# Performance work log

Hardware: AMD Instinct MI355X
Metric: run time of the kernel (lower is better)

## Reference

```python
import jax, jax.numpy as jnp
import numpy as np

B, T, E, K, NNEG = 128, 512, 128, 4, 64


def setup_inputs() -> dict:
    key = jax.random.key(0)
    k1, k2, k3, k4 = jax.random.split(key, 4)
    base_payload = jax.random.normal(k1, (B, T, E), dtype=jnp.float32)
    mapped_ctx_payload = jax.random.normal(k2, (B, T, E, K), dtype=jnp.float32)
    seq_lens = jax.random.randint(k3, (B,), 1, T + 1, dtype=jnp.int32)
    # valid positions mask over the flattened (B*T) pool of possible negatives
    valid = (jnp.arange(T)[None, :] < seq_lens[:, None]).reshape(-1)  # [B*T]
    logits = jnp.where(valid, 0.0, -1e30)[None, :]                    # [1, B*T]
    logits = jnp.broadcast_to(logits, (B, B * T))
    # mirrors torch.multinomial(mask, n_negatives): one draw set per batch row
    sample_ids = jax.random.categorical(k4, logits, shape=(NNEG, B)).T.astype(jnp.int32)
    return {
        "base_payload": base_payload,
        "mapped_ctx_payload": mapped_ctx_payload,
        "seq_lens": seq_lens,
        "sample_ids": sample_ids,
    }


def reference(base_payload, mapped_ctx_payload, seq_lens, sample_ids):
    b, t, e = base_payload.shape
    n_steps = mapped_ctx_payload.shape[-1]
    # length mask [b, t]
    len_mask = (jnp.arange(t)[None, :] < seq_lens[:, None]).astype(base_payload.dtype)
    # zero context embeddings past each sequence's length
    trimmed_mce = mapped_ctx_payload * len_mask[:, :, None, None]  # [b, t, e, n_steps]
    # gather sampled negatives from the flattened base embedding pool
    neg_samples = base_payload.reshape(b * t, e)[sample_ids]  # [b, n_neg, e]

    step_losses = []
    for i in range(1, n_steps + 1):
        ce_i = trimmed_mce[:, : t - i, :, i - 1]   # [b, t-i, e]
        be_i = base_payload[:, i:]                  # [b, t-i, e]
        positive_pred = jnp.sum(ce_i * be_i, axis=-1)             # [b, t-i]
        neg_pred = jnp.einsum('bse,bne->bsn', ce_i, neg_samples)  # [b, t-i, n_neg]
        logits = jnp.concatenate([positive_pred[..., None], neg_pred], axis=-1)
        step_losses.append(-jax.nn.log_softmax(logits, axis=-1)[:, :, 0].mean())
    return jnp.stack(step_losses).mean()
```

## Files before the change

### kernel.cpp

```cpp
#include <hip/hip_runtime.h>
#include <math.h>

#define NB 128
#define NT 512
#define NEDIM 128
#define NNEG 64
#define SCHUNK 16
#define CPB 4
#define SBLK (SCHUNK * CPB)
#define NXBLK (NT / SBLK)
#define NBLKS (NB * NXBLK)
#define WSN (NBLKS * 4)

typedef __bf16 bf16x8 __attribute__((ext_vector_type(8)));
typedef float  f32x4  __attribute__((ext_vector_type(4)));

__device__ __forceinline__ bf16x8 pack8(float4 v0, float4 v1) {
    bf16x8 o;
    o[0] = (__bf16)v0.x; o[1] = (__bf16)v0.y; o[2] = (__bf16)v0.z; o[3] = (__bf16)v0.w;
    o[4] = (__bf16)v1.x; o[5] = (__bf16)v1.y; o[6] = (__bf16)v1.z; o[7] = (__bf16)v1.w;
    return o;
}

__device__ __forceinline__ float chunk_const(int s0c) {
    const float wgt[4] = {1.f/261632.f, 1.f/261120.f, 1.f/260608.f, 1.f/260096.f};
    const float LOG65 = 4.1743873f;
    float c = 0.f;
    #pragma unroll
    for (int i = 1; i <= 4; ++i) {
        int hi = min(SCHUNK, (NT - i) - s0c);
        if (hi > 0) c += (float)hi * LOG65 * wgt[i - 1];
    }
    return c;
}

__launch_bounds__(256, 2)
__global__ void cpc_mfma_kernel(const float* __restrict__ base,
                                const float* __restrict__ mce,
                                const int*  __restrict__ seq_lens,
                                const int*  __restrict__ sample_ids,
                                float* __restrict__ ws)
{
    const int b    = blockIdx.y;
    const int s0   = blockIdx.x * SBLK;
    const int slot = (b * NXBLK + blockIdx.x) * 4;
    const int L    = seq_lens[b];
    const float LOG65 = 4.1743873f;
    const float wgt[4] = {1.f/261632.f, 1.f/261120.f, 1.f/260608.f, 1.f/260096.f};

    if (s0 >= L) {
        if (threadIdx.x < 4) {
            float c = 0.f;
            if (threadIdx.x == 0) {
                #pragma unroll
                for (int cc = 0; cc < CPB; ++cc) c += chunk_const(s0 + cc * SCHUNK);
            }
            ws[slot + threadIdx.x] = c;
        }
        return;
    }

    __shared__ __align__(16) __bf16 Afrag[2][1024 * 8];
    __shared__ __align__(16) __bf16 Bfrag[1024 * 8];
    __shared__ __align__(16) __bf16 Pfrag[2][512 * 8];

    const int tid  = threadIdx.x;
    const int lane = tid & 63;
    const int w    = tid >> 6;
    const int q    = lane >> 4;
    const int fl   = lane & 15;

    const float4* mce4  = (const float4*)mce;
    const float4* base4 = (const float4*)base;

    #pragma unroll
    for (int it = 0; it < 4; ++it) {
        int h  = tid + 256 * it;
        int n  = h >> 4;
        int eb = h & 15;
        int r  = sample_ids[b * NNEG + n];
        const float4* srcb = base4 + (size_t)r * (NEDIM / 4) + eb * 2;
        float4 v0 = srcb[0], v1 = srcb[1];
        *(bf16x8*)(&Bfrag[(size_t)((eb * 64 + n) ^ (eb & 7)) * 8]) = pack8(v0, v1);
    }

    const int sA  = tid & 15;
    const int ebA = tid >> 4;
    const int CsS = (ebA >> 2) * 4 + (sA >> 2);
    const int bcA = CsS * 64 + (ebA & 3) * 16 + (sA & 3) * 4;
    const int xA  = CsS & 7;

    {
        const float4* src = mce4 + (size_t)(b * NT + s0 + sA) * NEDIM + ebA * 8;
        float4 v[8];
        #pragma unroll
        for (int u = 0; u < 8; ++u) v[u] = src[u];
        const float* vf = (const float*)v;
        #pragma unroll
        for (int k = 0; k < 4; ++k) {
            bf16x8 o;
            #pragma unroll
            for (int u = 0; u < 8; ++u) o[u] = (__bf16)vf[4 * u + k];
            *(bf16x8*)(&Afrag[0][(size_t)((bcA + k) ^ xA) * 8]) = o;
        }
        #pragma unroll
        for (int it = 0; it < 2; ++it) {
            int h = tid + 256 * it;
            int j = h >> 4, ebP = h & 15;
            int srow = s0 + 1 + j; if (srow > NT - 1) srow = NT - 1;
            const float4* srcp = base4 + (size_t)(b * NT + srow) * (NEDIM / 4) + ebP * 2;
            *(bf16x8*)(&Pfrag[0][(size_t)((ebP * 32 + j) ^ (ebP & 7)) * 8]) = pack8(srcp[0], srcp[1]);
        }
    }
    __syncthreads();

    float lossacc = 0.f;
    const int sloc = w * 4 + q;

    for (int c = 0; c < CPB; ++c) {
        const int s0c = s0 + c * SCHUNK;
        const bool vcur  = (s0c < L);
        const bool vnext = (c + 1 < CPB) && (s0 + (c + 1) * SCHUNK < L);

        float4 av[8];
        float4 pv0a, pv0b, pv1a, pv1b;
        if (vnext) {
            const int s0n = s0c + SCHUNK;
            const float4* src = mce4 + (size_t)(b * NT + s0n + sA) * NEDIM + ebA * 8;
            #pragma unroll
            for (int u = 0; u < 8; ++u) av[u] = src[u];
            {
                int j = tid >> 4, ebP = tid & 15;
                int srow = s0n + 1 + j; if (srow > NT - 1) srow = NT - 1;
                const float4* srcp = base4 + (size_t)(b * NT + srow) * (NEDIM / 4) + ebP * 2;
                pv0a = srcp[0]; pv0b = srcp[1];
            }
            {
                int h = tid + 256;
                int j = h >> 4, ebP = h & 15;
                int srow = s0n + 1 + j; if (srow > NT - 1) srow = NT - 1;
                const float4* srcp = base4 + (size_t)(b * NT + srow) * (NEDIM / 4) + ebP * 2;
                pv1a = srcp[0]; pv1b = srcp[1];
            }
        }

        if (vcur) {
            const __bf16* Ab = Afrag[c & 1];
            const __bf16* Pb = Pfrag[c & 1];
            f32x4 acc[6];
            #pragma unroll
            for (int nt = 0; nt < 6; ++nt) acc[nt] = (f32x4){0.f, 0.f, 0.f, 0.f};

            #pragma unroll
            for (int kstep = 0; kstep < 4; ++kstep) {
                int CsA = kstep * 4 + w;
                bf16x8 af = *(const bf16x8*)(&Ab[(size_t)(((CsA * 64 + lane) ^ (CsA & 7))) * 8]);
                int ebB = kstep * 4 + q;
                int xb  = ebB & 7;
                bf16x8 bv[6];
                #pragma unroll
                for (int nt = 0; nt < 4; ++nt)
                    bv[nt] = *(const bf16x8*)(&Bfrag[(size_t)(((ebB * 64 + nt * 16 + fl) ^ xb)) * 8]);
                #pragma unroll
                for (int t = 0; t < 2; ++t)
                    bv[4 + t] = *(const bf16x8*)(&Pb[(size_t)(((ebB * 32 + t * 16 + fl) ^ xb)) * 8]);
                #pragma unroll
                for (int nt = 0; nt < 6; ++nt)
                    acc[nt] = __builtin_amdgcn_mfma_f32_16x16x32_bf16(af, bv[nt], acc[nt], 0, 0, 0);
            }

            const int sg = s0c + sloc;
            #pragma unroll
            for (int r = 0; r < 4; ++r) {
                int ip   = r + 1;
                int pcol = sloc + r;
                float z0 = acc[0][r], z1 = acc[1][r];
                float z2 = acc[2][r], z3 = acc[3][r];
                float pv = (pcol < 16) ? acc[4][r] : acc[5][r];
                float p  = __shfl(pv, (lane & 48) | (pcol & 15));
                float mx = fmaxf(fmaxf(z0, z1), fmaxf(z2, z3));
                mx = fmaxf(mx, __shfl_xor(mx, 1));
                mx = fmaxf(mx, __shfl_xor(mx, 2));
                mx = fmaxf(mx, __shfl_xor(mx, 4));
                mx = fmaxf(mx, __shfl_xor(mx, 8));
                mx = fmaxf(mx, p);
                float es = __expf(z0 - mx) + __expf(z1 - mx)
                         + __expf(z2 - mx) + __expf(z3 - mx);
                es += __shfl_xor(es, 1);
                es += __shfl_xor(es, 2);
                es += __shfl_xor(es, 4);
                es += __shfl_xor(es, 8);
                es += __expf(p - mx);
                float loss = __logf(es) + (mx - p);
                loss = (sg < L) ? loss : LOG65;
                bool take = (sg < NT - ip) && (fl == 0);
                lossacc += take ? wgt[r] * loss : 0.f;
            }
        } else if (tid == 0) {
            lossacc += chunk_const(s0c);
        }
        __syncthreads();

        if (vnext) {
            __bf16* An = Afrag[(c + 1) & 1];
            __bf16* Pn = Pfrag[(c + 1) & 1];
            const float* vf = (const float*)av;
            #pragma unroll
            for (int k = 0; k < 4; ++k) {
                bf16x8 o;
                #pragma unroll
                for (int u = 0; u < 8; ++u) o[u] = (__bf16)vf[4 * u + k];
                *(bf16x8*)(&An[(size_t)((bcA + k) ^ xA) * 8]) = o;
            }
            {
                int j = tid >> 4, ebP = tid & 15;
                *(bf16x8*)(&Pn[(size_t)((ebP * 32 + j) ^ (ebP & 7)) * 8]) = pack8(pv0a, pv0b);
            }
            {
                int h = tid + 256;
                int j = h >> 4, ebP = h & 15;
                *(bf16x8*)(&Pn[(size_t)((ebP * 32 + j) ^ (ebP & 7)) * 8]) = pack8(pv1a, pv1b);
            }
        }
        __syncthreads();
    }

    lossacc += __shfl_xor(lossacc, 16);
    lossacc += __shfl_xor(lossacc, 32);
    if (lane == 0) ws[slot + w] = lossacc;
}

__global__ void reduce_k(const float* __restrict__ ws, float* __restrict__ out) {
    const int tid = threadIdx.x;
    float s = 0.f;
    #pragma unroll
    for (int i = 0; i < WSN / 256; ++i) s += ws[tid + 256 * i];
    s += __shfl_xor(s, 1);
    s += __shfl_xor(s, 2);
    s += __shfl_xor(s, 4);
    s += __shfl_xor(s, 8);
    s += __shfl_xor(s, 16);
    s += __shfl_xor(s, 32);
    __shared__ float wsum[4];
    if ((tid & 63) == 0) wsum[tid >> 6] = s;
    __syncthreads();
    if (tid == 0) out[0] = wsum[0] + wsum[1] + wsum[2] + wsum[3];
}

extern "C" void kernel_launch(void* const* d_in, const int* in_sizes, int n_in,
                              void* d_out, int out_size, void* d_ws, size_t ws_size,
                              hipStream_t stream) {
    (void)in_sizes; (void)n_in; (void)out_size; (void)ws_size;
    const float* base       = (const float*)d_in[0];
    const float* mce        = (const float*)d_in[1];
    const int*   seq_lens   = (const int*)d_in[2];
    const int*   sample_ids = (const int*)d_in[3];
    float* out = (float*)d_out;
    float* ws  = (float*)d_ws;

    dim3 grid(NXBLK, NB);
    cpc_mfma_kernel<<<grid, 256, 0, stream>>>(base, mce, seq_lens, sample_ids, ws);
    reduce_k<<<1, 256, 0, stream>>>(ws, out);
}
```

Baseline: 224.7 us.

## Halve chunks per block, single-buffer LDS, and raise occupancy to four blocks

Reduces each block from four 16-row chunks to two, which doubles the grid and halves the work per block. Replaces the double-buffered A/P LDS tiles with single buffers and raises launch bounds to four blocks per CU, aiming for more concurrent waves to hide memory latency. The second chunk's mce load is still issued before the first chunk's compute, but the positive-row loads are now done after it. The gathered negative tile is loaded twice as often across the grid, and the tighter register budget may cause spills.

```diff
diff --git a/kernel.cpp b/kernel.cpp
--- a/kernel.cpp
+++ b/kernel.cpp
@@ -6,7 +6,7 @@
 #define NEDIM 128
 #define NNEG 64
 #define SCHUNK 16
-#define CPB 4
+#define CPB 2
 #define SBLK (SCHUNK * CPB)
 #define NXBLK (NT / SBLK)
 #define NBLKS (NB * NXBLK)
@@ -34,7 +34,69 @@
     return c;
 }
 
-__launch_bounds__(256, 2)
+__device__ __forceinline__ float compute_chunk(
+    const __bf16* __restrict__ Af, const __bf16* __restrict__ Bf,
+    const __bf16* __restrict__ Pf,
+    int s0c, int L, int lane, int w, int q, int fl)
+{
+    const float LOG65 = 4.1743873f;
+    const float wgt[4] = {1.f/261632.f, 1.f/261120.f, 1.f/260608.f, 1.f/260096.f};
+
+    f32x4 acc[6];
+    #pragma unroll
+    for (int nt = 0; nt < 6; ++nt) acc[nt] = (f32x4){0.f, 0.f, 0.f, 0.f};
+
+    #pragma unroll
+    for (int kstep = 0; kstep < 4; ++kstep) {
+        int CsA = kstep * 4 + w;
+        bf16x8 af = *(const bf16x8*)(&Af[(size_t)(((CsA * 64 + lane) ^ (CsA & 7))) * 8]);
+        int ebB = kstep * 4 + q;
+        int xb  = ebB & 7;
+        bf16x8 bv[6];
+        #pragma unroll
+        for (int nt = 0; nt < 4; ++nt)
+            bv[nt] = *(const bf16x8*)(&Bf[(size_t)(((ebB * 64 + nt * 16 + fl) ^ xb)) * 8]);
+        #pragma unroll
+        for (int t = 0; t < 2; ++t)
+            bv[4 + t] = *(const bf16x8*)(&Pf[(size_t)(((ebB * 32 + t * 16 + fl) ^ xb)) * 8]);
+        #pragma unroll
+        for (int nt = 0; nt < 6; ++nt)
+            acc[nt] = __builtin_amdgcn_mfma_f32_16x16x32_bf16(af, bv[nt], acc[nt], 0, 0, 0);
+    }
+
+    const int sloc = w * 4 + q;
+    const int sg   = s0c + sloc;
+    float lossacc = 0.f;
+    #pragma unroll
+    for (int r = 0; r < 4; ++r) {
+        int ip   = r + 1;
+        int pcol = sloc + r;
+        float z0 = acc[0][r], z1 = acc[1][r];
+        float z2 = acc[2][r], z3 = acc[3][r];
+        float pv = (pcol < 16) ? acc[4][r] : acc[5][r];
+        float p  = __shfl(pv, (lane & 48) | (pcol & 15));
+        float mx = fmaxf(fmaxf(z0, z1), fmaxf(z2, z3));
+        mx = fmaxf(mx, __shfl_xor(mx, 1));
+        mx = fmaxf(mx, __shfl_xor(mx, 2));
+        mx = fmaxf(mx, __shfl_xor(mx, 4));
+        mx = fmaxf(mx, __shfl_xor(mx, 8));
+        mx = fmaxf(mx, p);
+        float es = __expf(z0 - mx) + __expf(z1 - mx)
+                 + __expf(z2 - mx) + __expf(z3 - mx);
+        es += __shfl_xor(es, 1);
+        es += __shfl_xor(es, 2);
+        es += __shfl_xor(es, 4);
+        es += __shfl_xor(es, 8);
+        es += __expf(p - mx);
+        float loss = __logf(es) + (mx - p);
+        loss = (sg < L) ? loss : LOG65;
+        bool take = (sg < NT - ip) && (fl == 0);
+        lossacc += take ? wgt[r] * loss : 0.f;
+    }
+    return lossacc;
+}
+
+__launch_bounds__(256, 4)
 __global__ void cpc_mfma_kernel(const float* __restrict__ base,
                                 const float* __restrict__ mce,
                                 const int*  __restrict__ seq_lens,
@@ -45,24 +107,19 @@
     const int s0   = blockIdx.x * SBLK;
     const int slot = (b * NXBLK + blockIdx.x) * 4;
     const int L    = seq_lens[b];
-    const float LOG65 = 4.1743873f;
-    const float wgt[4] = {1.f/261632.f, 1.f/261120.f, 1.f/260608.f, 1.f/260096.f};
 
     if (s0 >= L) {
         if (threadIdx.x < 4) {
-            float c = 0.f;
-            if (threadIdx.x == 0) {
-                #pragma unroll
-                for (int cc = 0; cc < CPB; ++cc) c += chunk_const(s0 + cc * SCHUNK);
-            }
+            float c = (threadIdx.x == 0)
+                    ? chunk_const(s0) + chunk_const(s0 + SCHUNK) : 0.f;
             ws[slot + threadIdx.x] = c;
         }
         return;
     }
 
-    __shared__ __align__(16) __bf16 Afrag[2][1024 * 8];
+    __shared__ __align__(16) __bf16 Afrag[1024 * 8];
     __shared__ __align__(16) __bf16 Bfrag[1024 * 8];
-    __shared__ __align__(16) __bf16 Pfrag[2][512 * 8];
+    __shared__ __align__(16) __bf16 Pfrag[512 * 8];
 
     const int tid  = threadIdx.x;
     const int lane = tid & 63;
@@ -101,128 +158,55 @@
             bf16x8 o;
             #pragma unroll
             for (int u = 0; u < 8; ++u) o[u] = (__bf16)vf[4 * u + k];
-            *(bf16x8*)(&Afrag[0][(size_t)((bcA + k) ^ xA) * 8]) = o;
-        }
-        #pragma unroll
-        for (int it = 0; it < 2; ++it) {
-            int h = tid + 256 * it;
-            int j = h >> 4, ebP = h & 15;
-            int srow = s0 + 1 + j; if (srow > NT - 1) srow = NT - 1;
-            const float4* srcp = base4 + (size_t)(b * NT + srow) * (NEDIM / 4) + ebP * 2;
-            *(bf16x8*)(&Pfrag[0][(size_t)((ebP * 32 + j) ^ (ebP & 7)) * 8]) = pack8(srcp[0], srcp[1]);
-        }
+            *(bf16x8*)(&Afrag[(size_t)((bcA + k) ^ xA) * 8]) = o;
+        }
+    }
+    #pragma unroll
+    for (int it = 0; it < 2; ++it) {
+        int h = tid + 256 * it;
+        int j = h >> 4, ebP = h & 15;
+        int srow = s0 + 1 + j; if (srow > NT - 1) srow = NT - 1;
+        const float4* srcp = base4 + (size_t)(b * NT + srow) * (NEDIM / 4) + ebP * 2;
+        *(bf16x8*)(&Pfrag[(size_t)((ebP * 32 + j) ^ (ebP & 7)) * 8]) = pack8(srcp[0], srcp[1]);
     }
     __syncthreads();
 
-    float lossacc = 0.f;
-    const int sloc = w * 4 + q;
-
-    for (int c = 0; c < CPB; ++c) {
-        const int s0c = s0 + c * SCHUNK;
-        const bool vcur  = (s0c < L);
-        const bool vnext = (c + 1 < CPB) && (s0 + (c + 1) * SCHUNK < L);
-
-        float4 av[8];
-        float4 pv0a, pv0b, pv1a, pv1b;
-        if (vnext) {
-            const int s0n = s0c + SCHUNK;
-            const float4* src = mce4 + (size_t)(b * NT + s0n + sA) * NEDIM + ebA * 8;
-            #pragma unroll
-            for (int u = 0; u < 8; ++u) av[u] = src[u];
-            {
-                int j = tid >> 4, ebP = tid & 15;
-                int srow = s0n + 1 + j; if (srow > NT - 1) srow = NT - 1;
-                const float4* srcp = base4 + (size_t)(b * NT + srow) * (NEDIM / 4) + ebP * 2;
-                pv0a = srcp[0]; pv0b = srcp[1];
-            }
-            {
-                int h = tid + 256;
-                int j = h >> 4, ebP = h & 15;
-                int srow = s0n + 1 + j; if (srow > NT - 1) srow = NT - 1;
-                const float4* srcp = base4 + (size_t)(b * NT + srow) * (NEDIM / 4) + ebP * 2;
-                pv1a = srcp[0]; pv1b = srcp[1];
-            }
-        }
-
-        if (vcur) {
-            const __bf16* Ab = Afrag[c & 1];
-            const __bf16* Pb = Pfrag[c & 1];
-            f32x4 acc[6];
-            #pragma unroll
-            for (int nt = 0; nt < 6; ++nt) acc[nt] = (f32x4){0.f, 0.f, 0.f, 0.f};
-
-            #pragma unroll
-            for (int kstep = 0; kstep < 4; ++kstep) {
-                int CsA = kstep * 4 + w;
-                bf16x8 af = *(const bf16x8*)(&Ab[(size_t)(((CsA * 64 + lane) ^ (CsA & 7))) * 8]);
-                int ebB = kstep * 4 + q;
-                int xb  = ebB & 7;
-                bf16x8 bv[6];
-                #pragma unroll
-                for (int nt = 0; nt < 4; ++nt)
-                    bv[nt] = *(const bf16x8*)(&Bfrag[(size_t)(((ebB * 64 + nt * 16 + fl) ^ xb)) * 8]);
-                #pragma unroll
-                for (int t = 0; t < 2; ++t)
-                    bv[4 + t] = *(const bf16x8*)(&Pb[(size_t)(((ebB * 32 + t * 16 + fl) ^ xb)) * 8]);
-                #pragma unroll
-                for (int nt = 0; nt < 6; ++nt)
-                    acc[nt] = __builtin_amdgcn_mfma_f32_16x16x32_bf16(af, bv[nt], acc[nt], 0, 0, 0);
-            }
-
-            const int sg = s0c + sloc;
-            #pragma unroll
-            for (int r = 0; r < 4; ++r) {
-                int ip   = r + 1;
-                int pcol = sloc + r;
-                float z0 = acc[0][r], z1 = acc[1][r];
-                float z2 = acc[2][r], z3 = acc[3][r];
-                float pv = (pcol < 16) ? acc[4][r] : acc[5][r];
-                float p  = __shfl(pv, (lane & 48) | (pcol & 15));
-                float mx = fmaxf(fmaxf(z0, z1), fmaxf(z2, z3));
-                mx = fmaxf(mx, __shfl_xor(mx, 1));
-                mx = fmaxf(mx, __shfl_xor(mx, 2));
-                mx = fmaxf(mx, __shfl_xor(mx, 4));
-                mx = fmaxf(mx, __shfl_xor(mx, 8));
-                mx = fmaxf(mx, p);
-                float es = __expf(z0 - mx) + __expf(z1 - mx)
-                         + __expf(z2 - mx) + __expf(z3 - mx);
-                es += __shfl_xor(es, 1);
-                es += __shfl_xor(es, 2);
-                es += __shfl_xor(es, 4);
-                es += __shfl_xor(es, 8);
-                es += __expf(p - mx);
-                float loss = __logf(es) + (mx - p);
-                loss = (sg < L) ? loss : LOG65;
-                bool take = (sg < NT - ip) && (fl == 0);
-                lossacc += take ? wgt[r] * loss : 0.f;
-            }
-        } else if (tid == 0) {
-            lossacc += chunk_const(s0c);
-        }
+    const int  s1 = s0 + SCHUNK;
+    const bool v1 = (s1 < L);
+
+    float4 av[8];
+    if (v1) {
+        const float4* src = mce4 + (size_t)(b * NT + s1 + sA) * NEDIM + ebA * 8;
+        #pragma unroll
+        for (int u = 0; u < 8; ++u) av[u] = src[u];
+    }
+
+    float lossacc = compute_chunk(Afrag, Bfrag, Pfrag, s0, L, lane, w, q, fl);
+
+    if (v1) {
         __syncthreads();
-
-        if (vnext) {
-            __bf16* An = Afrag[(c + 1) & 1];
-            __bf16* Pn = Pfrag[(c + 1) & 1];
+        {
             const float* vf = (const float*)av;
             #pragma unroll
             for (int k = 0; k < 4; ++k) {
                 bf16x8 o;
                 #pragma unroll
                 for (int u = 0; u < 8; ++u) o[u] = (__bf16)vf[4 * u + k];
-                *(bf16x8*)(&An[(size_t)((bcA + k) ^ xA) * 8]) = o;
+                *(bf16x8*)(&Afrag[(size_t)((bcA + k) ^ xA) * 8]) = o;
             }
-            {
-                int j = tid >> 4, ebP = tid & 15;
-                *(bf16x8*)(&Pn[(size_t)((ebP * 32 + j) ^ (ebP & 7)) * 8]) = pack8(pv0a, pv0b);
-            }
-            {
-                int h = tid + 256;
-                int j = h >> 4, ebP = h & 15;
-                *(bf16x8*)(&Pn[(size_t)((ebP * 32 + j) ^ (ebP & 7)) * 8]) = pack8(pv1a, pv1b);
-            }
+        }
+        #pragma unroll
+        for (int it = 0; it < 2; ++it) {
+            int h = tid + 256 * it;
+            int j = h >> 4, ebP = h & 15;
+            int srow = s1 + 1 + j; if (srow > NT - 1) srow = NT - 1;
+            const float4* srcp = base4 + (size_t)(b * NT + srow) * (NEDIM / 4) + ebP * 2;
+            *(bf16x8*)(&Pfrag[(size_t)((ebP * 32 + j) ^ (ebP & 7)) * 8]) = pack8(srcp[0], srcp[1]);
         }
         __syncthreads();
+        lossacc += compute_chunk(Afrag, Bfrag, Pfrag, s1, L, lane, w, q, fl);
+    } else if (tid == 0) {
+        lossacc += chunk_const(s1);
     }
 
     lossacc += __shfl_xor(lossacc, 16);
```

Result: faster. 212.1 us (-5.6%).
